# Kernel tuning notes

Measured on AMD Instinct MI355X. Metric: run time of the kernel, lower is better.

Reference implementation:

```python
import jax, jax.numpy as jnp
import numpy as np

NUM_Q = 8      # num_quantizers
K = 1024       # codebook_size (num_tokens)
D = 512        # feature dim
B, T = 16, 2000
BETA = 0.25    # commitment weight


def setup_inputs() -> dict:
    key = jax.random.key(0)
    kx, kc = jax.random.split(key)
    x = jax.random.normal(kx, (B, T, D), dtype=jnp.float32)
    # learned codebooks, one per quantizer stage: [NUM_Q, K, D]
    codebooks = jax.random.normal(kc, (NUM_Q, K, D), dtype=jnp.float32)
    return {"x": x, "codebooks": codebooks}


def _vq_stage(residual, codebook):
    """Single VQ layer: nearest-codeword search + straight-through + commitment loss.
    residual: [B, T, D]; codebook: [K, D]."""
    sg = jax.lax.stop_gradient
    # squared L2 distances via ||r||^2 - 2 r.e + ||e||^2  -> [B, T, K]
    r2 = jnp.sum(residual * residual, axis=-1, keepdims=True)          # [B,T,1]
    e2 = jnp.sum(codebook * codebook, axis=-1)                          # [K]
    dots = jnp.einsum('btd,kd->btk', residual, codebook)                # [B,T,K]
    dist = r2 - 2.0 * dots + e2
    indices = jnp.argmin(dist, axis=-1)                                 # [B,T] int
    quantized = codebook[indices]                                       # [B,T,D] gather
    # commitment + codebook loss (VQ-VAE style)
    loss = (BETA * jnp.mean((sg(quantized) - residual) ** 2)
            + jnp.mean((quantized - sg(residual)) ** 2))
    # straight-through estimator
    quantized_st = residual + sg(quantized - residual)
    return quantized_st, indices, loss


def reference(x, codebooks):
    def step(carry, codebook):
        residual, q_out = carry
        q, idx, loss = _vq_stage(residual, codebook)
        residual = residual - jax.lax.stop_gradient(q)
        return (residual, q_out + q), (idx, loss)

    init = (x, jnp.zeros_like(x))
    (_, quantized_out), (all_indices, all_losses) = jax.lax.scan(step, init, codebooks)
    # all_indices: [NUM_Q, B, T]; mean loss across stages
    return quantized_out, all_indices, jnp.mean(all_losses)
```

## Files before the change

kernel.cpp:

```cpp
#include <hip/hip_runtime.h>

#define M_TOK 32000
#define DIM   512
#define KCB   1024
#define NQ    8
#define BM 64
#define BN 256
#define KS 16

typedef _Float16 f16x8 __attribute__((ext_vector_type(8)));
typedef _Float16 f16x4 __attribute__((ext_vector_type(4)));
typedef float f32x4 __attribute__((ext_vector_type(4)));

#define FENCE() __builtin_amdgcn_sched_barrier(0)
#define WAIT_VM(N) asm volatile("s_waitcnt vmcnt(" #N ")" ::: "memory")
#define WAIT_LGKM0() asm volatile("s_waitcnt lgkmcnt(0)" ::: "memory")

__device__ __forceinline__ void gload_lds16(const void* g, void* l) {
  __builtin_amdgcn_global_load_lds(
      (const __attribute__((address_space(1))) unsigned int*)g,
      (__attribute__((address_space(3))) unsigned int*)l, 16, 0, 0);
}

__device__ __forceinline__ float wave_reduce_sum(float v) {
#pragma unroll
  for (int off = 32; off > 0; off >>= 1) v += __shfl_xor(v, off, 64);
  return v;
}

__device__ __forceinline__ unsigned int fenc(float f) {
  unsigned int u = __float_as_uint(f);
  return (u & 0x80000000u) ? ~u : (u | 0x80000000u);
}

__global__ __launch_bounds__(256) void rvq_init_kernel(
    const float* __restrict__ x, const float* __restrict__ cb,
    float* __restrict__ e2, float* __restrict__ r2,
    unsigned long long* __restrict__ keys, float* __restrict__ lossCell) {
  if (blockIdx.x == 0 && threadIdx.x == 0) *lossCell = 0.f;
  for (int i = blockIdx.x * 256 + threadIdx.x; i < M_TOK; i += gridDim.x * 256)
    keys[i] = ~0ull;
  int row = blockIdx.x * 4 + (threadIdx.x >> 6);
  int lane = threadIdx.x & 63;
  const float* src;
  float* dst;
  if (row < NQ * KCB) {
    src = cb + (size_t)row * DIM;
    dst = e2 + row;
  } else {
    int t = row - NQ * KCB;
    if (t >= M_TOK) return;
    src = x + (size_t)t * DIM;
    dst = r2 + t;
  }
  const float4* s4 = (const float4*)src;
  float s = 0.f;
  float4 v = s4[lane];
  s += v.x * v.x + v.y * v.y + v.z * v.z + v.w * v.w;
  v = s4[lane + 64];
  s += v.x * v.x + v.y * v.y + v.z * v.z + v.w * v.w;
  s = wave_reduce_sum(s);
  if (lane == 0) *dst = s;
}

__global__ __launch_bounds__(256) void rvq_split_cb_kernel(
    const float* __restrict__ cb, _Float16* __restrict__ cbF) {
  int gid = blockIdx.x * 256 + threadIdx.x;
  if (gid >= NQ * 16 * 4 * 4 * 4 * 64) return;
  int lane = gid & 63;
  int nf = (gid >> 6) & 3;
  int w  = (gid >> 8) & 3;
  int nc = (gid >> 10) & 3;
  int ks = (gid >> 12) & 15;
  int s  = gid >> 16;
  int col = nc * 256 + w * 64 + nf * 16 + (lane & 15);
  int kbase = ks * 32 + (lane >> 4) * 8;
  const float* src = cb + ((size_t)s * KCB + col) * DIM + kbase;
  f16x8 h, l;
#pragma unroll
  for (int j = 0; j < 8; ++j) {
    float v = src[j];
    _Float16 hh = (_Float16)v;
    h[j] = hh;
    l[j] = (_Float16)(v - (float)hh);
  }
  size_t base = ((((size_t)((s * 16 + ks) * 4 + nc) * 4 + w) * 8 + nf * 2) * 64
                 + lane) * 8;
  *(f16x8*)(cbF + base) = h;
  *(f16x8*)(cbF + base + 512) = l;
}

__global__ __launch_bounds__(256, 2) void rvq_argmin_kernel(
    const float* __restrict__ rin,
    const _Float16* __restrict__ cbF,
    const float* __restrict__ e2,
    const float* __restrict__ r2,
    unsigned long long* __restrict__ keys) {
  __shared__ __align__(16) _Float16 bufB[2][4][8][512];
  __shared__ __align__(16) _Float16 bufA[2][4][2][512];

  const int tid = threadIdx.x;
  const int lane = tid & 63, w = tid >> 6;
  const int l15 = lane & 15, l4 = lane >> 4;
  const int x = blockIdx.x & 7, i = blockIdx.x >> 3;
  const int nc = x >> 1;
  const int m = (x & 1) * 250 + i;
  const int m0 = m * BM;
  const int c0 = nc * BN;

  const _Float16* gB = cbF + (((size_t)nc * 4 + w) * 8) * 512 + (size_t)lane * 8;
  const int p0 = tid, p1 = tid + 256;

  f32x4 acc[4][4];
#pragma unroll
  for (int a = 0; a < 4; ++a)
#pragma unroll
    for (int b = 0; b < 4; ++b) acc[a][b] = (f32x4){0.f, 0.f, 0.f, 0.f};

  float4 a0, a1;
  auto ldA = [&](int ks, int p) {
    return *(const float4*)(rin + (size_t)(m0 + (p >> 3)) * DIM + ks * 32 + (p & 7) * 4);
  };
  auto cvtWriteA = [&](int buf, const float4& v, int p) {
    int r = p >> 3, kg = p & 7;
    int mf = r >> 4, lp = (kg >> 1) * 16 + (r & 15), fo = (kg & 1) * 4;
    float vv[4] = {v.x, v.y, v.z, v.w};
    f16x4 h, l;
#pragma unroll
    for (int j = 0; j < 4; ++j) {
      _Float16 hh = (_Float16)vv[j];
      h[j] = hh;
      l[j] = (_Float16)(vv[j] - (float)hh);
    }
    *(f16x4*)&bufA[buf][mf][0][lp * 8 + fo] = h;
    *(f16x4*)&bufA[buf][mf][1][lp * 8 + fo] = l;
  };
  a0 = ldA(0, p0);
  a1 = ldA(0, p1);
  FENCE();
#pragma unroll
  for (int c = 0; c < 8; ++c)
    gload_lds16(gB + c * 512, &bufB[0][w][c][0]);
  WAIT_VM(8);
  FENCE();
  cvtWriteA(0, a0, p0);
  cvtWriteA(0, a1, p1);

  for (int ks = 0; ks < KS; ++ks) {
    const int cur = ks & 1;
    if (ks < KS - 1) {
      a0 = ldA(ks + 1, p0);
      a1 = ldA(ks + 1, p1);
      FENCE();
      const _Float16* gBs = gB + (size_t)(ks + 1) * 65536;
#pragma unroll
      for (int c = 0; c < 8; ++c)
        gload_lds16(gBs + c * 512, &bufB[cur ^ 1][w][c][0]);
      WAIT_VM(10);
    } else {
      WAIT_VM(0);
    }
    FENCE();
    WAIT_LGKM0();
    FENCE();
    __builtin_amdgcn_s_barrier();
    FENCE();
    f16x8 ah[4], al[4];
#pragma unroll
    for (int mf = 0; mf < 4; ++mf) {
      ah[mf] = *(const f16x8*)&bufA[cur][mf][0][lane * 8];
      al[mf] = *(const f16x8*)&bufA[cur][mf][1][lane * 8];
    }
    __builtin_amdgcn_s_setprio(1);
#pragma unroll
    for (int nf = 0; nf < 4; ++nf) {
      f16x8 bh = *(const f16x8*)&bufB[cur][w][nf * 2][lane * 8];
      f16x8 bl = *(const f16x8*)&bufB[cur][w][nf * 2 + 1][lane * 8];
#pragma unroll
      for (int mf = 0; mf < 4; ++mf) {
        acc[mf][nf] = __builtin_amdgcn_mfma_f32_16x16x32_f16(ah[mf], bh, acc[mf][nf], 0, 0, 0);
        acc[mf][nf] = __builtin_amdgcn_mfma_f32_16x16x32_f16(ah[mf], bl, acc[mf][nf], 0, 0, 0);
        acc[mf][nf] = __builtin_amdgcn_mfma_f32_16x16x32_f16(al[mf], bh, acc[mf][nf], 0, 0, 0);
      }
    }
    __builtin_amdgcn_s_setprio(0);
    if (ks < KS - 1) {
      cvtWriteA(cur ^ 1, a0, p0);
      cvtWriteA(cur ^ 1, a1, p1);
    }
  }

  float rv[4][4];
#pragma unroll
  for (int mf = 0; mf < 4; ++mf) {
    float4 q = *(const float4*)(r2 + m0 + mf * 16 + l4 * 4);
    rv[mf][0] = q.x; rv[mf][1] = q.y; rv[mf][2] = q.z; rv[mf][3] = q.w;
  }
  float minv[16];
  int mini[16];
#pragma unroll
  for (int i2 = 0; i2 < 16; ++i2) { minv[i2] = 3.4e38f; mini[i2] = 0; }
#pragma unroll
  for (int nf = 0; nf < 4; ++nf) {
    int col = c0 + w * 64 + nf * 16 + l15;
    float e2v = e2[col];
#pragma unroll
    for (int mf = 0; mf < 4; ++mf) {
#pragma unroll
      for (int rr = 0; rr < 4; ++rr) {
        float d = (rv[mf][rr] - 2.f * acc[mf][nf][rr]) + e2v;
        int ii = mf * 4 + rr;
        if (d < minv[ii]) { minv[ii] = d; mini[ii] = col; }
      }
    }
  }
#pragma unroll
  for (int mf = 0; mf < 4; ++mf) {
#pragma unroll
    for (int rr = 0; rr < 4; ++rr) {
      int ii = mf * 4 + rr;
      float v = minv[ii];
      int ix = mini[ii];
#pragma unroll
      for (int off = 8; off; off >>= 1) {
        float ov = __shfl_xor(v, off, 16);
        int oi = __shfl_xor(ix, off, 16);
        if (ov < v || (ov == v && oi < ix)) { v = ov; ix = oi; }
      }
      if (l15 == 0) {
        int tok = m0 + mf * 16 + l4 * 4 + rr;
        unsigned long long key = ((unsigned long long)fenc(v) << 32) | (unsigned)ix;
        atomicMin(&keys[tok], key);
      }
    }
  }
}

__global__ __launch_bounds__(256) void rvq_update_kernel(
    const float* __restrict__ rin, const float* __restrict__ cb,
    unsigned long long* __restrict__ keys,
    float* __restrict__ rout, float* __restrict__ r2out,
    float* __restrict__ idx_out, float* __restrict__ lossCell) {
  const int wave = threadIdx.x >> 6, lane = threadIdx.x & 63;
  __shared__ float lred[4];
  float lpart = 0.f;
  for (int r = wave; r < 64; r += 4) {
    const int tok = blockIdx.x * 64 + r;
    const unsigned idx = (unsigned)(keys[tok] & 0xffffffffu);
    const float4* rrow = (const float4*)(rin + (size_t)tok * DIM);
    const float4* crow = (const float4*)(cb + (size_t)idx * DIM);
    float4* orow = (float4*)(rout + (size_t)tok * DIM);
    float ssq_t = 0.f, ssq_r = 0.f;
#pragma unroll
    for (int c4 = 0; c4 < 2; ++c4) {
      int c = lane + c4 * 64;
      float4 a = rrow[c], q = crow[c];
      float4 t = make_float4(q.x - a.x, q.y - a.y, q.z - a.z, q.w - a.w);
      float4 qst = make_float4(a.x + t.x, a.y + t.y, a.z + t.z, a.w + t.w);
      float4 rn = make_float4(a.x - qst.x, a.y - qst.y, a.z - qst.z, a.w - qst.w);
      orow[c] = rn;
      ssq_t += t.x * t.x + t.y * t.y + t.z * t.z + t.w * t.w;
      ssq_r += rn.x * rn.x + rn.y * rn.y + rn.z * rn.z + rn.w * rn.w;
    }
    float tot_t = wave_reduce_sum(ssq_t);
    float tot_r = wave_reduce_sum(ssq_r);
    if (lane == 0) {
      idx_out[tok] = (float)idx;
      keys[tok] = ~0ull;
      r2out[tok] = tot_r;
      lpart += tot_t;
    }
  }
  if (lane == 0) lred[wave] = lpart;
  __syncthreads();
  if (threadIdx.x == 0)
    atomicAdd(lossCell, lred[0] + lred[1] + lred[2] + lred[3]);
}

__global__ __launch_bounds__(256) void rvq_finalize_kernel(
    const float* __restrict__ x, float* __restrict__ out,
    const float* __restrict__ lossCell, float* __restrict__ loss_out) {
  size_t i = (size_t)blockIdx.x * 256 + threadIdx.x;
  const size_t n4 = (size_t)M_TOK * DIM / 4;
  if (i < n4) {
    const float4* x4 = (const float4*)x;
    float4* o4 = (float4*)out;
    float4 a = x4[i], r = o4[i];
    o4[i] = make_float4(a.x - r.x, a.y - r.y, a.z - r.z, a.w - r.w);
  }
  if (blockIdx.x == 0 && threadIdx.x == 0) {
    *loss_out = *lossCell * (1.25f / 131072000.f);
  }
}

extern "C" void kernel_launch(void* const* d_in, const int* in_sizes, int n_in,
                              void* d_out, int out_size, void* d_ws, size_t ws_size,
                              hipStream_t stream) {
  const float* x = (const float*)d_in[0];
  const float* cb = (const float*)d_in[1];
  float* out = (float*)d_out;
  float* idx_out = out + (size_t)M_TOK * DIM;
  float* loss_out = idx_out + (size_t)NQ * M_TOK;

  char* wsp = (char*)d_ws;
  unsigned long long* keys = (unsigned long long*)wsp;
  float* e2 = (float*)(wsp + 256000);
  float* r2 = (float*)(wsp + 288768);
  float* lossCell = (float*)(wsp + 416768);
  _Float16* cbF = (_Float16*)(wsp + 416800 + 224);

  {
    int rows = NQ * KCB + M_TOK;
    rvq_init_kernel<<<(rows + 3) / 4, 256, 0, stream>>>(x, cb, e2, r2, keys, lossCell);
    rvq_split_cb_kernel<<<NQ * 16 * 4 * 4 * 4 * 64 / 256, 256, 0, stream>>>(cb, cbF);
  }
  float* resbuf = out;
  const size_t stageF = (size_t)16 * 4 * 4 * 8 * 512;
  for (int s = 0; s < NQ; ++s) {
    const float* rin = (s == 0) ? x : resbuf;
    rvq_argmin_kernel<<<(M_TOK / BM) * 4, 256, 0, stream>>>(
        rin, cbF + (size_t)s * stageF, e2 + s * KCB, r2, keys);
    rvq_update_kernel<<<M_TOK / 64, 256, 0, stream>>>(
        rin, cb + (size_t)s * KCB * DIM, keys, resbuf, r2,
        idx_out + (size_t)s * M_TOK, lossCell);
  }
  rvq_finalize_kernel<<<(M_TOK * DIM / 4 + 255) / 256, 256, 0, stream>>>(
      x, out, lossCell, loss_out);
}
```

Baseline: 1.284 ms.

## Precompute fp16 hi/lo residual splits and load MFMA operands directly to registers

The residual is now split into fp16 hi/lo arrays once, in the init and update kernels, instead of being converted inside the argmin kernel. The argmin kernel drops LDS staging and barriers and loads A and B fragments straight from global memory into a register double buffer, using a codebook layout rearranged for that access. The block-to-tile mapping also changes. The goal is to remove LDS traffic, synchronisation and in-loop conversion, at the cost of more global and L2 traffic, extra workspace, and extra fp16 writes in the update kernel.

Result: slower. 1.587 ms (+23.6%).

```diff
diff --git a/kernel.cpp b/kernel.cpp
--- a/kernel.cpp
+++ b/kernel.cpp
@@ -5,23 +5,12 @@
 #define KCB   1024
 #define NQ    8
 #define BM 64
-#define BN 256
 #define KS 16
 
 typedef _Float16 f16x8 __attribute__((ext_vector_type(8)));
 typedef _Float16 f16x4 __attribute__((ext_vector_type(4)));
 typedef float f32x4 __attribute__((ext_vector_type(4)));
 
-#define FENCE() __builtin_amdgcn_sched_barrier(0)
-#define WAIT_VM(N) asm volatile("s_waitcnt vmcnt(" #N ")" ::: "memory")
-#define WAIT_LGKM0() asm volatile("s_waitcnt lgkmcnt(0)" ::: "memory")
-
-__device__ __forceinline__ void gload_lds16(const void* g, void* l) {
-  __builtin_amdgcn_global_load_lds(
-      (const __attribute__((address_space(1))) unsigned int*)g,
-      (__attribute__((address_space(3))) unsigned int*)l, 16, 0, 0);
-}
-
 __device__ __forceinline__ float wave_reduce_sum(float v) {
 #pragma unroll
   for (int off = 32; off > 0; off >>= 1) v += __shfl_xor(v, off, 64);
@@ -33,161 +22,138 @@
   return (u & 0x80000000u) ? ~u : (u | 0x80000000u);
 }
 
+__device__ __forceinline__ _Float16 hi16(float v) { return (_Float16)v; }
+__device__ __forceinline__ _Float16 lo16(float v, _Float16 h) {
+  return (_Float16)(v - (float)h);
+}
+
+struct Split4 { f16x4 h, l; };
+__device__ __forceinline__ Split4 split4(float4 v) {
+  Split4 s;
+  s.h[0] = hi16(v.x); s.l[0] = lo16(v.x, s.h[0]);
+  s.h[1] = hi16(v.y); s.l[1] = lo16(v.y, s.h[1]);
+  s.h[2] = hi16(v.z); s.l[2] = lo16(v.z, s.h[2]);
+  s.h[3] = hi16(v.w); s.l[3] = lo16(v.w, s.h[3]);
+  return s;
+}
+
 __global__ __launch_bounds__(256) void rvq_init_kernel(
     const float* __restrict__ x, const float* __restrict__ cb,
     float* __restrict__ e2, float* __restrict__ r2,
-    unsigned long long* __restrict__ keys, float* __restrict__ lossCell) {
+    unsigned long long* __restrict__ keys, float* __restrict__ lossCell,
+    _Float16* __restrict__ ahi, _Float16* __restrict__ alo) {
   if (blockIdx.x == 0 && threadIdx.x == 0) *lossCell = 0.f;
   for (int i = blockIdx.x * 256 + threadIdx.x; i < M_TOK; i += gridDim.x * 256)
     keys[i] = ~0ull;
   int row = blockIdx.x * 4 + (threadIdx.x >> 6);
   int lane = threadIdx.x & 63;
-  const float* src;
-  float* dst;
   if (row < NQ * KCB) {
-    src = cb + (size_t)row * DIM;
-    dst = e2 + row;
+    const float4* s4 = (const float4*)(cb + (size_t)row * DIM);
+    float s = 0.f;
+    float4 v = s4[lane];
+    s += v.x * v.x + v.y * v.y + v.z * v.z + v.w * v.w;
+    v = s4[lane + 64];
+    s += v.x * v.x + v.y * v.y + v.z * v.z + v.w * v.w;
+    s = wave_reduce_sum(s);
+    if (lane == 0) e2[row] = s;
   } else {
     int t = row - NQ * KCB;
     if (t >= M_TOK) return;
-    src = x + (size_t)t * DIM;
-    dst = r2 + t;
-  }
-  const float4* s4 = (const float4*)src;
-  float s = 0.f;
-  float4 v = s4[lane];
-  s += v.x * v.x + v.y * v.y + v.z * v.z + v.w * v.w;
-  v = s4[lane + 64];
-  s += v.x * v.x + v.y * v.y + v.z * v.z + v.w * v.w;
-  s = wave_reduce_sum(s);
-  if (lane == 0) *dst = s;
+    const float4* s4 = (const float4*)(x + (size_t)t * DIM);
+    float4 v0 = s4[lane], v1 = s4[lane + 64];
+    float s = v0.x * v0.x + v0.y * v0.y + v0.z * v0.z + v0.w * v0.w
+            + v1.x * v1.x + v1.y * v1.y + v1.z * v1.z + v1.w * v1.w;
+    Split4 s0 = split4(v0), s1 = split4(v1);
+    size_t base = (size_t)t * DIM + lane * 4;
+    *(f16x4*)(ahi + base) = s0.h;
+    *(f16x4*)(alo + base) = s0.l;
+    *(f16x4*)(ahi + base + 256) = s1.h;
+    *(f16x4*)(alo + base + 256) = s1.l;
+    s = wave_reduce_sum(s);
+    if (lane == 0) r2[t] = s;
+  }
 }
 
 __global__ __launch_bounds__(256) void rvq_split_cb_kernel(
-    const float* __restrict__ cb, _Float16* __restrict__ cbF) {
+    const float* __restrict__ cb, _Float16* __restrict__ cbhF,
+    _Float16* __restrict__ cblF) {
   int gid = blockIdx.x * 256 + threadIdx.x;
-  if (gid >= NQ * 16 * 4 * 4 * 4 * 64) return;
-  int lane = gid & 63;
-  int nf = (gid >> 6) & 3;
-  int w  = (gid >> 8) & 3;
-  int nc = (gid >> 10) & 3;
-  int ks = (gid >> 12) & 15;
-  int s  = gid >> 16;
-  int col = nc * 256 + w * 64 + nf * 16 + (lane & 15);
-  int kbase = ks * 32 + (lane >> 4) * 8;
-  const float* src = cb + ((size_t)s * KCB + col) * DIM + kbase;
-  f16x8 h, l;
+  int l = gid & 63;
+  int c = (gid >> 6) & 15;
+  int F = (gid >> 10) & 63;
+  int s = gid >> 16;
+  if (s >= NQ) return;
+  const float* src = cb + (size_t)(s * KCB + F * 16 + (l & 15)) * DIM
+                        + c * 32 + (l >> 4) * 8;
+  f16x8 h, lo;
 #pragma unroll
   for (int j = 0; j < 8; ++j) {
-    float v = src[j];
-    _Float16 hh = (_Float16)v;
+    _Float16 hh = hi16(src[j]);
     h[j] = hh;
-    l[j] = (_Float16)(v - (float)hh);
-  }
-  size_t base = ((((size_t)((s * 16 + ks) * 4 + nc) * 4 + w) * 8 + nf * 2) * 64
-                 + lane) * 8;
-  *(f16x8*)(cbF + base) = h;
-  *(f16x8*)(cbF + base + 512) = l;
+    lo[j] = lo16(src[j], hh);
+  }
+  *(f16x8*)(cbhF + (size_t)gid * 8) = h;
+  *(f16x8*)(cblF + (size_t)gid * 8) = lo;
 }
 
 __global__ __launch_bounds__(256, 2) void rvq_argmin_kernel(
-    const float* __restrict__ rin,
-    const _Float16* __restrict__ cbF,
+    const _Float16* __restrict__ ahi,
+    const _Float16* __restrict__ alo,
+    const _Float16* __restrict__ cbhF,
+    const _Float16* __restrict__ cblF,
     const float* __restrict__ e2,
     const float* __restrict__ r2,
     unsigned long long* __restrict__ keys) {
-  __shared__ __align__(16) _Float16 bufB[2][4][8][512];
-  __shared__ __align__(16) _Float16 bufA[2][4][2][512];
-
   const int tid = threadIdx.x;
   const int lane = tid & 63, w = tid >> 6;
   const int l15 = lane & 15, l4 = lane >> 4;
-  const int x = blockIdx.x & 7, i = blockIdx.x >> 3;
-  const int nc = x >> 1;
-  const int m = (x & 1) * 250 + i;
-  const int m0 = m * BM;
-  const int c0 = nc * BN;
-
-  const _Float16* gB = cbF + (((size_t)nc * 4 + w) * 8) * 512 + (size_t)lane * 8;
-  const int p0 = tid, p1 = tid + 256;
-
+  const int m = blockIdx.x >> 2, nc = blockIdx.x & 3;
+  const int m0 = m * BM, c0 = nc * 256;
+
+  const _Float16* aH = ahi + (size_t)(m0 + l15) * DIM + l4 * 8;
+  const _Float16* aL = alo + (size_t)(m0 + l15) * DIM + l4 * 8;
+  const int Fb = nc * 16 + w * 4;
+  const _Float16* bH = cbhF + ((size_t)Fb * 16 * 64 + lane) * 8;
+  const _Float16* bL = cblF + ((size_t)Fb * 16 * 64 + lane) * 8;
+
+  f16x8 Ab[2][8], Bb[2][8];
   f32x4 acc[4][4];
 #pragma unroll
   for (int a = 0; a < 4; ++a)
 #pragma unroll
     for (int b = 0; b < 4; ++b) acc[a][b] = (f32x4){0.f, 0.f, 0.f, 0.f};
 
-  float4 a0, a1;
-  auto ldA = [&](int ks, int p) {
-    return *(const float4*)(rin + (size_t)(m0 + (p >> 3)) * DIM + ks * 32 + (p & 7) * 4);
+  auto loadA = [&](int buf, int ks) {
+#pragma unroll
+    for (int mf = 0; mf < 4; ++mf) {
+      Ab[buf][mf]     = *(const f16x8*)(aH + (size_t)mf * 16 * DIM + ks * 32);
+      Ab[buf][4 + mf] = *(const f16x8*)(aL + (size_t)mf * 16 * DIM + ks * 32);
+    }
   };
-  auto cvtWriteA = [&](int buf, const float4& v, int p) {
-    int r = p >> 3, kg = p & 7;
-    int mf = r >> 4, lp = (kg >> 1) * 16 + (r & 15), fo = (kg & 1) * 4;
-    float vv[4] = {v.x, v.y, v.z, v.w};
-    f16x4 h, l;
-#pragma unroll
-    for (int j = 0; j < 4; ++j) {
-      _Float16 hh = (_Float16)vv[j];
-      h[j] = hh;
-      l[j] = (_Float16)(vv[j] - (float)hh);
-    }
-    *(f16x4*)&bufA[buf][mf][0][lp * 8 + fo] = h;
-    *(f16x4*)&bufA[buf][mf][1][lp * 8 + fo] = l;
+  auto loadB = [&](int buf, int ks) {
+#pragma unroll
+    for (int nf = 0; nf < 4; ++nf) {
+      Bb[buf][nf]     = *(const f16x8*)(bH + (size_t)(nf * 16 + ks) * 512);
+      Bb[buf][4 + nf] = *(const f16x8*)(bL + (size_t)(nf * 16 + ks) * 512);
+    }
   };
-  a0 = ldA(0, p0);
-  a1 = ldA(0, p1);
-  FENCE();
-#pragma unroll
-  for (int c = 0; c < 8; ++c)
-    gload_lds16(gB + c * 512, &bufB[0][w][c][0]);
-  WAIT_VM(8);
-  FENCE();
-  cvtWriteA(0, a0, p0);
-  cvtWriteA(0, a1, p1);
-
+  loadA(0, 0); loadB(0, 0);
+  loadA(1, 1); loadB(1, 1);
+#pragma unroll
   for (int ks = 0; ks < KS; ++ks) {
-    const int cur = ks & 1;
-    if (ks < KS - 1) {
-      a0 = ldA(ks + 1, p0);
-      a1 = ldA(ks + 1, p1);
-      FENCE();
-      const _Float16* gBs = gB + (size_t)(ks + 1) * 65536;
-#pragma unroll
-      for (int c = 0; c < 8; ++c)
-        gload_lds16(gBs + c * 512, &bufB[cur ^ 1][w][c][0]);
-      WAIT_VM(10);
-    } else {
-      WAIT_VM(0);
-    }
-    FENCE();
-    WAIT_LGKM0();
-    FENCE();
-    __builtin_amdgcn_s_barrier();
-    FENCE();
-    f16x8 ah[4], al[4];
-#pragma unroll
-    for (int mf = 0; mf < 4; ++mf) {
-      ah[mf] = *(const f16x8*)&bufA[cur][mf][0][lane * 8];
-      al[mf] = *(const f16x8*)&bufA[cur][mf][1][lane * 8];
-    }
+    const int b = ks & 1;
     __builtin_amdgcn_s_setprio(1);
 #pragma unroll
     for (int nf = 0; nf < 4; ++nf) {
-      f16x8 bh = *(const f16x8*)&bufB[cur][w][nf * 2][lane * 8];
-      f16x8 bl = *(const f16x8*)&bufB[cur][w][nf * 2 + 1][lane * 8];
 #pragma unroll
       for (int mf = 0; mf < 4; ++mf) {
-        acc[mf][nf] = __builtin_amdgcn_mfma_f32_16x16x32_f16(ah[mf], bh, acc[mf][nf], 0, 0, 0);
-        acc[mf][nf] = __builtin_amdgcn_mfma_f32_16x16x32_f16(ah[mf], bl, acc[mf][nf], 0, 0, 0);
-        acc[mf][nf] = __builtin_amdgcn_mfma_f32_16x16x32_f16(al[mf], bh, acc[mf][nf], 0, 0, 0);
+        acc[mf][nf] = __builtin_amdgcn_mfma_f32_16x16x32_f16(Ab[b][mf], Bb[b][nf], acc[mf][nf], 0, 0, 0);
+        acc[mf][nf] = __builtin_amdgcn_mfma_f32_16x16x32_f16(Ab[b][mf], Bb[b][4 + nf], acc[mf][nf], 0, 0, 0);
+        acc[mf][nf] = __builtin_amdgcn_mfma_f32_16x16x32_f16(Ab[b][4 + mf], Bb[b][nf], acc[mf][nf], 0, 0, 0);
       }
     }
     __builtin_amdgcn_s_setprio(0);
-    if (ks < KS - 1) {
-      cvtWriteA(cur ^ 1, a0, p0);
-      cvtWriteA(cur ^ 1, a1, p1);
-    }
+    if (ks + 2 < KS) { loadA(b, ks + 2); loadB(b, ks + 2); }
   }
 
   float rv[4][4];
@@ -240,7 +206,8 @@
     const float* __restrict__ rin, const float* __restrict__ cb,
     unsigned long long* __restrict__ keys,
     float* __restrict__ rout, float* __restrict__ r2out,
-    float* __restrict__ idx_out, float* __restrict__ lossCell) {
+    float* __restrict__ idx_out, float* __restrict__ lossCell,
+    _Float16* __restrict__ ahi, _Float16* __restrict__ alo) {
   const int wave = threadIdx.x >> 6, lane = threadIdx.x & 63;
   __shared__ float lred[4];
   float lpart = 0.f;
@@ -259,6 +226,9 @@
       float4 qst = make_float4(a.x + t.x, a.y + t.y, a.z + t.z, a.w + t.w);
       float4 rn = make_float4(a.x - qst.x, a.y - qst.y, a.z - qst.z, a.w - qst.w);
       orow[c] = rn;
+      Split4 sp = split4(rn);
+      *(f16x4*)(ahi + (size_t)tok * DIM + c * 4) = sp.h;
+      *(f16x4*)(alo + (size_t)tok * DIM + c * 4) = sp.l;
       ssq_t += t.x * t.x + t.y * t.y + t.z * t.z + t.w * t.w;
       ssq_r += rn.x * rn.x + rn.y * rn.y + rn.z * rn.z + rn.w * rn.w;
     }
@@ -304,25 +274,29 @@
 
   char* wsp = (char*)d_ws;
   unsigned long long* keys = (unsigned long long*)wsp;
-  float* e2 = (float*)(wsp + 256000);
-  float* r2 = (float*)(wsp + 288768);
-  float* lossCell = (float*)(wsp + 416768);
-  _Float16* cbF = (_Float16*)(wsp + 416800 + 224);
+  float* e2 = (float*)(wsp + 262144);
+  float* r2 = (float*)(wsp + 294912);
+  float* lossCell = (float*)(wsp + 425984);
+  _Float16* cbhF = (_Float16*)(wsp + 524288);
+  _Float16* cblF = (_Float16*)(wsp + 524288 + 8388608);
+  _Float16* ahi = (_Float16*)(wsp + 524288 + 16777216);
+  _Float16* alo = ahi + (size_t)M_TOK * DIM;
 
   {
     int rows = NQ * KCB + M_TOK;
-    rvq_init_kernel<<<(rows + 3) / 4, 256, 0, stream>>>(x, cb, e2, r2, keys, lossCell);
-    rvq_split_cb_kernel<<<NQ * 16 * 4 * 4 * 4 * 64 / 256, 256, 0, stream>>>(cb, cbF);
+    rvq_init_kernel<<<(rows + 3) / 4, 256, 0, stream>>>(x, cb, e2, r2, keys,
+                                                        lossCell, ahi, alo);
+    rvq_split_cb_kernel<<<NQ * 64 * 16 * 64 / 256, 256, 0, stream>>>(cb, cbhF, cblF);
   }
   float* resbuf = out;
-  const size_t stageF = (size_t)16 * 4 * 4 * 8 * 512;
   for (int s = 0; s < NQ; ++s) {
     const float* rin = (s == 0) ? x : resbuf;
     rvq_argmin_kernel<<<(M_TOK / BM) * 4, 256, 0, stream>>>(
-        rin, cbF + (size_t)s * stageF, e2 + s * KCB, r2, keys);
+        ahi, alo, cbhF + (size_t)s * KCB * DIM, cblF + (size_t)s * KCB * DIM,
+        e2 + s * KCB, r2, keys);
     rvq_update_kernel<<<M_TOK / 64, 256, 0, stream>>>(
         rin, cb + (size_t)s * KCB * DIM, keys, resbuf, r2,
-        idx_out + (size_t)s * M_TOK, lossCell);
+        idx_out + (size_t)s * M_TOK, lossCell, ahi, alo);
   }
   rvq_finalize_kernel<<<(M_TOK * DIM / 4 + 255) / 256, 256, 0, stream>>>(
       x, out, lossCell, loss_out);
```
